# Performance work log

Hardware: AMD Instinct MI355X
Metric: run time of the kernel (lower is better)

Reference implementation:

```python
import jax, jax.numpy as jnp
import numpy as np

N_NODES = 50000
N_EDGES = 800000
FEAT = 128


def setup_inputs() -> dict:
    key = jax.random.key(0)
    k1, k2, k3, k4 = jax.random.split(key, 4)
    x = jax.random.normal(k1, (N_NODES, FEAT), dtype=jnp.float32)
    a = jax.random.normal(k2, (FEAT, 1), dtype=jnp.float32) * (1.414 / np.sqrt(FEAT))
    row = jax.random.randint(k3, (N_EDGES,), 0, N_NODES, dtype=jnp.int64)
    col = jax.random.randint(k4, (N_EDGES,), 0, N_NODES, dtype=jnp.int64)
    return {"x": x, "a": a, "row": row, "col": col}


def reference(x, a, row, col):
    n = x.shape[0]
    # per-node score e = x @ a, squeezed to [N]
    e = jnp.squeeze(x @ a, axis=-1)
    # gather per-edge score from the destination (column) node, as in e[col]
    vals = e[col]                                            # [E]
    # sparse row-wise softmax (numerically stable via segment max)
    m = jax.ops.segment_max(vals, row, num_segments=n)       # [N]
    m = jnp.where(jnp.isfinite(m), m, 0.0)                   # empty rows -> 0
    ex = jnp.exp(vals - m[row])                              # [E]
    denom = jax.ops.segment_sum(ex, row, num_segments=n)     # [N]
    att = ex / denom[row]                                    # [E]
    # sparse-dense matmul: h[i] = sum_j att_ij * x[j]
    h_prime = jax.ops.segment_sum(att[:, None] * x[col], row, num_segments=n)
    return h_prime
```

## Files before the change

### kernel.cpp

```cpp
#include <hip/hip_runtime.h>
#include <hip/hip_bf16.h>
#include <math.h>

#define FEAT 128

__device__ __forceinline__ int pack_bf162(float lo, float hi) {
    __hip_bfloat162 b = __float22bfloat162_rn(make_float2(lo, hi));
    union { __hip_bfloat162 b; int i; } u;
    u.b = b;
    return u.i;
}

__global__ void dot_hist_kernel(const float* __restrict__ x, const float* __restrict__ a,
                                const int* __restrict__ row,
                                float* __restrict__ exw, int* __restrict__ cnt,
                                int2* __restrict__ xh, int n, int nE) {
    int tid = blockIdx.x * blockDim.x + threadIdx.x;
    if (tid < nE) atomicAdd(&cnt[row[tid]], 1);
    int node = tid >> 5;
    int l = tid & 31;
    if (node >= n) return;
    float4 xv = ((const float4*)(x + (size_t)node * FEAT))[l];
    float4 av = ((const float4*)a)[l];
    int2 pk;
    pk.x = pack_bf162(xv.x, xv.y);
    pk.y = pack_bf162(xv.z, xv.w);
    xh[(size_t)node * 32 + l] = pk;
    float p = xv.x * av.x + xv.y * av.y + xv.z * av.z + xv.w * av.w;
    #pragma unroll
    for (int off = 16; off > 0; off >>= 1) p += __shfl_xor(p, off);
    if (l == 0) exw[node] = __expf(p);
}

__global__ void scanA_kernel(const int* __restrict__ cnt, int* __restrict__ rowptr,
                             int* __restrict__ bsum, int n) {
    __shared__ int smem[1024];
    int i = blockIdx.x * 1024 + threadIdx.x;
    int v = (i < n) ? cnt[i] : 0;
    smem[threadIdx.x] = v;
    __syncthreads();
    #pragma unroll
    for (int off = 1; off < 1024; off <<= 1) {
        int t = (threadIdx.x >= (unsigned)off) ? smem[threadIdx.x - off] : 0;
        __syncthreads();
        smem[threadIdx.x] += t;
        __syncthreads();
    }
    if (i < n) rowptr[i] = smem[threadIdx.x] - v;
    if (threadIdx.x == 1023) bsum[blockIdx.x] = smem[1023];
}

__global__ void scanB_kernel(const int* __restrict__ bsum, int* __restrict__ boff, int nb) {
    int lane = threadIdx.x;
    int v = (lane < nb) ? bsum[lane] : 0;
    #pragma unroll
    for (int off = 1; off < 64; off <<= 1) {
        int t = __shfl_up(v, off);
        if (lane >= off) v += t;
    }
    if (lane < nb) boff[lane + 1] = v;
    if (lane == 0) boff[0] = 0;
}

__global__ void scanC_kernel(int* __restrict__ rowptr, int* __restrict__ cursor,
                             const int* __restrict__ boff, int n, int nb) {
    int i = blockIdx.x * blockDim.x + threadIdx.x;
    if (i < n) {
        int v = rowptr[i] + boff[i >> 10];
        rowptr[i] = v;
        cursor[i] = v;
    }
    if (i == 0) rowptr[n] = boff[nb];
}

__global__ void fill_kernel(const int* __restrict__ row, const int* __restrict__ col,
                            int* __restrict__ cursor, unsigned short* __restrict__ ecol,
                            int nE) {
    int k = blockIdx.x * blockDim.x + threadIdx.x;
    if (k >= nE) return;
    int r = row[k];
    int c = col[k];
    int pos = atomicAdd(&cursor[r], 1);
    ecol[pos] = (unsigned short)c;
}

__global__ void gather_kernel(const __hip_bfloat162* __restrict__ xh,
                              const float* __restrict__ exw,
                              const int* __restrict__ rowptr,
                              const unsigned short* __restrict__ ecol,
                              float* __restrict__ h, int n) {
    __shared__ int2 sbuf[4][64];
    int wid = threadIdx.x >> 6;
    int node = (int)((blockIdx.x * blockDim.x + threadIdx.x) >> 6);
    int lane = threadIdx.x & 63;
    if (node >= n) return;
    int s = rowptr[node];
    int eend = rowptr[node + 1];
    float accx = 0.0f, accy = 0.0f, wsum = 0.0f;
    for (int base = s; base < eend; base += 64) {
        int idx = base + lane;
        if (idx < eend) {
            int c = (int)ecol[idx];
            float w = exw[c];
            sbuf[wid][lane] = make_int2(c << 6, __float_as_int(w));
        }
        int m = min(64, eend - base);
        int j = 0;
        for (; j + 4 <= m; j += 4) {
            int2 p0 = sbuf[wid][j + 0];
            int2 p1 = sbuf[wid][j + 1];
            int2 p2 = sbuf[wid][j + 2];
            int2 p3 = sbuf[wid][j + 3];
            float2 f0 = __bfloat1622float2(xh[p0.x + lane]);
            float2 f1 = __bfloat1622float2(xh[p1.x + lane]);
            float2 f2 = __bfloat1622float2(xh[p2.x + lane]);
            float2 f3 = __bfloat1622float2(xh[p3.x + lane]);
            float w0 = __int_as_float(p0.y), w1 = __int_as_float(p1.y);
            float w2 = __int_as_float(p2.y), w3 = __int_as_float(p3.y);
            accx += w0 * f0.x; accy += w0 * f0.y;
            accx += w1 * f1.x; accy += w1 * f1.y;
            accx += w2 * f2.x; accy += w2 * f2.y;
            accx += w3 * f3.x; accy += w3 * f3.y;
            wsum += w0 + w1 + w2 + w3;
        }
        for (; j < m; ++j) {
            int2 p = sbuf[wid][j];
            float2 f = __bfloat1622float2(xh[p.x + lane]);
            float w = __int_as_float(p.y);
            accx += w * f.x; accy += w * f.y; wsum += w;
        }
    }
    float inv = (eend > s) ? 1.0f / wsum : 0.0f;
    float2 out;
    out.x = accx * inv;
    out.y = accy * inv;
    ((float2*)(h + (size_t)node * FEAT))[lane] = out;
}

extern "C" void kernel_launch(void* const* d_in, const int* in_sizes, int n_in,
                              void* d_out, int out_size, void* d_ws, size_t ws_size,
                              hipStream_t stream) {
    const float* x = (const float*)d_in[0];
    const float* a = (const float*)d_in[1];
    const int* row = (const int*)d_in[2];
    const int* col = (const int*)d_in[3];
    int n  = in_sizes[0] / FEAT;
    int nE = in_sizes[2];
    float* h = (float*)d_out;
    int nb = (n + 1023) / 1024;

    char* p = (char*)d_ws;
    auto alloc = [&](size_t bytes) { char* q = p; p += (bytes + 15) & ~(size_t)15; return q; };
    int* cnt              = (int*)alloc((size_t)n * 4);
    int* cursor           = (int*)alloc((size_t)n * 4);
    float* exw            = (float*)alloc((size_t)n * 4);
    int* rowptr           = (int*)alloc((size_t)(n + 1) * 4);
    int* bsum             = (int*)alloc((size_t)nb * 4);
    int* boff             = (int*)alloc((size_t)(nb + 1) * 4);
    unsigned short* ecol  = (unsigned short*)alloc((size_t)nE * 2);
    int2* xh              = (int2*)alloc((size_t)n * 32 * 8);

    hipMemsetAsync(cnt, 0, (size_t)n * sizeof(int), stream);

    int t1 = (n * 32 > nE) ? n * 32 : nE;
    dot_hist_kernel<<<(t1 + 255) / 256, 256, 0, stream>>>(x, a, row, exw, cnt, xh, n, nE);
    scanA_kernel<<<nb, 1024, 0, stream>>>(cnt, rowptr, bsum, n);
    scanB_kernel<<<1, 64, 0, stream>>>(bsum, boff, nb);
    scanC_kernel<<<(n + 255) / 256, 256, 0, stream>>>(rowptr, cursor, boff, n, nb);
    fill_kernel<<<(nE + 255) / 256, 256, 0, stream>>>(row, col, cursor, ecol, nE);
    gather_kernel<<<(n + 3) / 4, 256, 0, stream>>>((const __hip_bfloat162*)xh, exw,
                                                   rowptr, ecol, h, n);
}
```

Before: 199.0 us.

## Fuse three-pass scan into single-pass lookback scan and widen fill/gather accesses

Replaces the three scan kernels with one kernel where each block publishes its total via flags and spins on predecessors' flags to get its prefix, removing two launches. The fill kernel processes two edges per thread with vector loads. The gather kernel computes the weight sum via a wave reduction and reads shared edge pairs as int4. The spin-wait relies on all earlier blocks being resident and on at most 64 blocks.

```diff
diff --git a/kernel.cpp b/kernel.cpp
--- a/kernel.cpp
+++ b/kernel.cpp
@@ -32,56 +32,69 @@
     if (l == 0) exw[node] = __expf(p);
 }
 
-__global__ void scanA_kernel(const int* __restrict__ cnt, int* __restrict__ rowptr,
-                             int* __restrict__ bsum, int n) {
-    __shared__ int smem[1024];
-    int i = blockIdx.x * 1024 + threadIdx.x;
-    int v = (i < n) ? cnt[i] : 0;
-    smem[threadIdx.x] = v;
+__global__ void scan_kernel(const int* __restrict__ cnt, int* __restrict__ rowptr,
+                            int* __restrict__ cursor, int* flags, int n, int nb) {
+    __shared__ int sm[256];
+    __shared__ int sprefix;
+    int b = blockIdx.x;
+    int i0 = (b << 10) + (int)threadIdx.x * 4;
+    int v0 = (i0 + 0 < n) ? cnt[i0 + 0] : 0;
+    int v1 = (i0 + 1 < n) ? cnt[i0 + 1] : 0;
+    int v2 = (i0 + 2 < n) ? cnt[i0 + 2] : 0;
+    int v3 = (i0 + 3 < n) ? cnt[i0 + 3] : 0;
+    int t4 = v0 + v1 + v2 + v3;
+    sm[threadIdx.x] = t4;
     __syncthreads();
     #pragma unroll
-    for (int off = 1; off < 1024; off <<= 1) {
-        int t = (threadIdx.x >= (unsigned)off) ? smem[threadIdx.x - off] : 0;
+    for (int off = 1; off < 256; off <<= 1) {
+        int u = (threadIdx.x >= (unsigned)off) ? sm[threadIdx.x - off] : 0;
         __syncthreads();
-        smem[threadIdx.x] += t;
+        sm[threadIdx.x] += u;
         __syncthreads();
     }
-    if (i < n) rowptr[i] = smem[threadIdx.x] - v;
-    if (threadIdx.x == 1023) bsum[blockIdx.x] = smem[1023];
-}
-
-__global__ void scanB_kernel(const int* __restrict__ bsum, int* __restrict__ boff, int nb) {
-    int lane = threadIdx.x;
-    int v = (lane < nb) ? bsum[lane] : 0;
-    #pragma unroll
-    for (int off = 1; off < 64; off <<= 1) {
-        int t = __shfl_up(v, off);
-        if (lane >= off) v += t;
+    if (threadIdx.x == 0)
+        __hip_atomic_store(&flags[b], sm[255] + 1, __ATOMIC_RELEASE,
+                           __HIP_MEMORY_SCOPE_AGENT);
+    if (threadIdx.x < 64) {
+        int lane = threadIdx.x;
+        int pred = 0;
+        if (lane < b) {
+            int f;
+            do {
+                f = __hip_atomic_load(&flags[lane], __ATOMIC_ACQUIRE,
+                                      __HIP_MEMORY_SCOPE_AGENT);
+            } while (f == 0);
+            pred = f - 1;
+        }
+        #pragma unroll
+        for (int off = 32; off > 0; off >>= 1) pred += __shfl_xor(pred, off);
+        if (lane == 0) sprefix = pred;
     }
-    if (lane < nb) boff[lane + 1] = v;
-    if (lane == 0) boff[0] = 0;
-}
-
-__global__ void scanC_kernel(int* __restrict__ rowptr, int* __restrict__ cursor,
-                             const int* __restrict__ boff, int n, int nb) {
-    int i = blockIdx.x * blockDim.x + threadIdx.x;
-    if (i < n) {
-        int v = rowptr[i] + boff[i >> 10];
-        rowptr[i] = v;
-        cursor[i] = v;
-    }
-    if (i == 0) rowptr[n] = boff[nb];
+    __syncthreads();
+    int base = sprefix + sm[threadIdx.x] - t4;
+    if (i0 + 0 < n) { rowptr[i0 + 0] = base;                cursor[i0 + 0] = base; }
+    if (i0 + 1 < n) { rowptr[i0 + 1] = base + v0;           cursor[i0 + 1] = base + v0; }
+    if (i0 + 2 < n) { rowptr[i0 + 2] = base + v0 + v1;      cursor[i0 + 2] = base + v0 + v1; }
+    if (i0 + 3 < n) { rowptr[i0 + 3] = base + v0 + v1 + v2; cursor[i0 + 3] = base + v0 + v1 + v2; }
+    if (b == nb - 1 && threadIdx.x == 255) rowptr[n] = sprefix + sm[255];
 }
 
 __global__ void fill_kernel(const int* __restrict__ row, const int* __restrict__ col,
                             int* __restrict__ cursor, unsigned short* __restrict__ ecol,
                             int nE) {
-    int k = blockIdx.x * blockDim.x + threadIdx.x;
-    if (k >= nE) return;
-    int r = row[k];
-    int c = col[k];
-    int pos = atomicAdd(&cursor[r], 1);
-    ecol[pos] = (unsigned short)c;
+    int k = (blockIdx.x * blockDim.x + threadIdx.x) * 2;
+    if (k + 1 < nE) {
+        int2 r2 = *(const int2*)(row + k);
+        int2 c2 = *(const int2*)(col + k);
+        int p0 = atomicAdd(&cursor[r2.x], 1);
+        ecol[p0] = (unsigned short)c2.x;
+        int p1 = atomicAdd(&cursor[r2.y], 1);
+        ecol[p1] = (unsigned short)c2.y;
+    } else if (k < nE) {
+        int r = row[k], c = col[k];
+        int p0 = atomicAdd(&cursor[r], 1);
+        ecol[p0] = (unsigned short)c;
+    }
 }
 
 __global__ void gather_kernel(const __hip_bfloat162* __restrict__ xh,
@@ -89,7 +102,7 @@
                               const int* __restrict__ rowptr,
                               const unsigned short* __restrict__ ecol,
                               float* __restrict__ h, int n) {
-    __shared__ int2 sbuf[4][64];
+    __shared__ __align__(16) int2 sbuf[4][64];
     int wid = threadIdx.x >> 6;
     int node = (int)((blockIdx.x * blockDim.x + threadIdx.x) >> 6);
     int lane = threadIdx.x & 63;
@@ -97,37 +110,39 @@
     int s = rowptr[node];
     int eend = rowptr[node + 1];
     float accx = 0.0f, accy = 0.0f, wsum = 0.0f;
+    const int4* sb4 = (const int4*)&sbuf[wid][0];
     for (int base = s; base < eend; base += 64) {
         int idx = base + lane;
+        float w = 0.0f;
         if (idx < eend) {
             int c = (int)ecol[idx];
-            float w = exw[c];
+            w = exw[c];
             sbuf[wid][lane] = make_int2(c << 6, __float_as_int(w));
         }
+        #pragma unroll
+        for (int off = 32; off > 0; off >>= 1) w += __shfl_xor(w, off);
+        wsum += w;
         int m = min(64, eend - base);
         int j = 0;
         for (; j + 4 <= m; j += 4) {
-            int2 p0 = sbuf[wid][j + 0];
-            int2 p1 = sbuf[wid][j + 1];
-            int2 p2 = sbuf[wid][j + 2];
-            int2 p3 = sbuf[wid][j + 3];
-            float2 f0 = __bfloat1622float2(xh[p0.x + lane]);
-            float2 f1 = __bfloat1622float2(xh[p1.x + lane]);
-            float2 f2 = __bfloat1622float2(xh[p2.x + lane]);
-            float2 f3 = __bfloat1622float2(xh[p3.x + lane]);
-            float w0 = __int_as_float(p0.y), w1 = __int_as_float(p1.y);
-            float w2 = __int_as_float(p2.y), w3 = __int_as_float(p3.y);
+            int4 q0 = sb4[(j >> 1) + 0];
+            int4 q1 = sb4[(j >> 1) + 1];
+            float2 f0 = __bfloat1622float2(xh[q0.x + lane]);
+            float2 f1 = __bfloat1622float2(xh[q0.z + lane]);
+            float2 f2 = __bfloat1622float2(xh[q1.x + lane]);
+            float2 f3 = __bfloat1622float2(xh[q1.z + lane]);
+            float w0 = __int_as_float(q0.y), w1 = __int_as_float(q0.w);
+            float w2 = __int_as_float(q1.y), w3 = __int_as_float(q1.w);
             accx += w0 * f0.x; accy += w0 * f0.y;
             accx += w1 * f1.x; accy += w1 * f1.y;
             accx += w2 * f2.x; accy += w2 * f2.y;
             accx += w3 * f3.x; accy += w3 * f3.y;
-            wsum += w0 + w1 + w2 + w3;
         }
         for (; j < m; ++j) {
             int2 p = sbuf[wid][j];
             float2 f = __bfloat1622float2(xh[p.x + lane]);
-            float w = __int_as_float(p.y);
-            accx += w * f.x; accy += w * f.y; wsum += w;
+            float wj = __int_as_float(p.y);
+            accx += wj * f.x; accy += wj * f.y;
         }
     }
     float inv = (eend > s) ? 1.0f / wsum : 0.0f;
@@ -151,23 +166,20 @@
 
     char* p = (char*)d_ws;
     auto alloc = [&](size_t bytes) { char* q = p; p += (bytes + 15) & ~(size_t)15; return q; };
-    int* cnt              = (int*)alloc((size_t)n * 4);
-    int* cursor           = (int*)alloc((size_t)n * 4);
-    float* exw            = (float*)alloc((size_t)n * 4);
-    int* rowptr           = (int*)alloc((size_t)(n + 1) * 4);
-    int* bsum             = (int*)alloc((size_t)nb * 4);
-    int* boff             = (int*)alloc((size_t)(nb + 1) * 4);
-    unsigned short* ecol  = (unsigned short*)alloc((size_t)nE * 2);
-    int2* xh              = (int2*)alloc((size_t)n * 32 * 8);
+    int* cnt             = (int*)alloc((size_t)n * 4);
+    int* flags           = (int*)alloc(64 * 4);
+    int* cursor          = (int*)alloc((size_t)n * 4);
+    float* exw           = (float*)alloc((size_t)n * 4);
+    int* rowptr          = (int*)alloc((size_t)(n + 1) * 4);
+    unsigned short* ecol = (unsigned short*)alloc((size_t)nE * 2);
+    int2* xh             = (int2*)alloc((size_t)n * 32 * 8);
 
-    hipMemsetAsync(cnt, 0, (size_t)n * sizeof(int), stream);
+    hipMemsetAsync(cnt, 0, ((size_t)n + 64) * sizeof(int), stream);
 
     int t1 = (n * 32 > nE) ? n * 32 : nE;
     dot_hist_kernel<<<(t1 + 255) / 256, 256, 0, stream>>>(x, a, row, exw, cnt, xh, n, nE);
-    scanA_kernel<<<nb, 1024, 0, stream>>>(cnt, rowptr, bsum, n);
-    scanB_kernel<<<1, 64, 0, stream>>>(bsum, boff, nb);
-    scanC_kernel<<<(n + 255) / 256, 256, 0, stream>>>(rowptr, cursor, boff, n, nb);
-    fill_kernel<<<(nE + 255) / 256, 256, 0, stream>>>(row, col, cursor, ecol, nE);
+    scan_kernel<<<nb, 256, 0, stream>>>(cnt, rowptr, cursor, flags, n, nb);
+    fill_kernel<<<(nE / 2 + 255) / 256, 256, 0, stream>>>(row, col, cursor, ecol, nE);
     gather_kernel<<<(n + 3) / 4, 256, 0, stream>>>((const __hip_bfloat162*)xh, exw,
                                                    rowptr, ecol, h, n);
 }
```

After: 199.5 us. Within noise of the previous version (+0.3%).
